# Kernel optimization log

Hardware: AMD Instinct MI355X
Metric: run time of the kernel (lower is better)

Reference implementation:

```python
import jax, jax.numpy as jnp
import numpy as np

BS, T, FIN, FOUT = 8, 1024, 512, 512
ALPHA = 0.1      # leaky relu slope
T_K = 3          # t_ksize (odd); temporal band radius = T_K // 2
S_K = 4          # s_ksize semantic topk
NEG_INF = -9e15


def setup_inputs() -> dict:
    key = jax.random.key(0)
    k1, k2, k3, k4 = jax.random.split(key, 4)
    # xavier-uniform-ish scales (gain 1.414)
    w_lim = 1.414 * np.sqrt(6.0 / (FIN + FOUT))
    a_lim = 1.414 * np.sqrt(6.0 / (2 * FOUT + 1))
    return {
        "x_a": jax.random.normal(k1, (BS, T, FIN), jnp.float32),
        "x_v": jax.random.normal(k2, (BS, T, FIN), jnp.float32),
        "W": jax.random.uniform(k3, (FIN, FOUT), jnp.float32, -w_lim, w_lim),
        "a": jax.random.uniform(k4, (2 * FOUT, 1), jnp.float32, -a_lim, a_lim),
    }


def _temporal_mask(t):
    # tem_adj[i,j] = 1 iff |i-j| <= T_K//2 and i, j on the same side of t-0.5
    idx = jnp.arange(2 * t)
    same_side = (idx[:, None] >= t) == (idx[None, :] >= t)
    band = jnp.abs(idx[:, None] - idx[None, :]) <= (T_K // 2)
    return band & same_side  # (2t, 2t) bool


def _semantic_block_mask(x, k):
    # x: (bs, t, d). Top-k neighbors by negative squared euclidean distance.
    inner = 2.0 * jnp.einsum("btd,bsd->bts", x, x)
    sq = jnp.sum(x * x, axis=-1, keepdims=True)  # (bs, t, 1)
    pd = -(sq - inner + jnp.swapaxes(sq, -1, -2))  # (bs, t, t)
    _, idx = jax.lax.top_k(pd, k)  # (bs, t, k)
    bs, t = x.shape[0], x.shape[1]
    b_ix = jnp.arange(bs)[:, None, None]
    r_ix = jnp.arange(t)[None, :, None]
    return jnp.zeros((bs, t, t), bool).at[b_ix, r_ix, idx].set(True)


def reference(x_a, x_v, W, a):
    bs, t, _ = x_a.shape
    h = jnp.concatenate([x_a, x_v], axis=1)          # (bs, 2t, FIN)
    Wh = h @ W                                        # (bs, 2t, FOUT)

    # additive GAT score: e = leakyrelu(Wh a1 + (Wh a2)^T)
    Wh1 = Wh @ a[:FOUT]                               # (bs, 2t, 1)
    Wh2 = Wh @ a[FOUT:]                               # (bs, 2t, 1)
    e = Wh1 + jnp.swapaxes(Wh2, -1, -2)               # (bs, 2t, 2t)
    e = jnp.where(e > 0, e, ALPHA * e)                # leaky relu

    # adjacency: temporal band + semantic topk within aa / vv blocks
    tem = _temporal_mask(t)                           # (2t, 2t)
    sem_aa = _semantic_block_mask(Wh[:, :t], S_K)     # (bs, t, t)
    sem_vv = _semantic_block_mask(Wh[:, t:], S_K)     # (bs, t, t)
    zb = jnp.zeros((bs, t, t), bool)
    sem = jnp.concatenate([
        jnp.concatenate([sem_aa, zb], axis=-1),
        jnp.concatenate([zb, sem_vv], axis=-1),
    ], axis=1)                                        # (bs, 2t, 2t)
    mask = tem[None] | sem

    attention = jax.nn.softmax(jnp.where(mask, e, NEG_INF), axis=-1)
    h_prime = jax.nn.elu(attention @ Wh)              # (bs, 2t, FOUT)
    return h_prime[:, :t], h_prime[:, t:]
```

## Files before the change

kernel.cpp:

```cpp
#include <hip/hip_runtime.h>
#include <math.h>

#define T_ 1024
#define BS_ 8
#define D_ 512
#define NROWS_ (BS_*2*T_)
#define ALPHA_ 0.1f

typedef _Float16 f16;
typedef _Float16 f16x8 __attribute__((ext_vector_type(8)));
typedef _Float16 f16x4 __attribute__((ext_vector_type(4)));
typedef _Float16 f16x2 __attribute__((ext_vector_type(2)));
typedef float f32x4 __attribute__((ext_vector_type(4)));

#define MFMA16(A,B,C) __builtin_amdgcn_mfma_f32_16x16x32_f16((A),(B),(C),0,0,0)

__device__ __forceinline__ void gl16(const void* g, void* l) {
    __builtin_amdgcn_global_load_lds(
        (const __attribute__((address_space(1))) unsigned int*)g,
        (__attribute__((address_space(3))) unsigned int*)l, 16, 0, 0);
}

#if __has_builtin(__builtin_amdgcn_fdot2)
__device__ __forceinline__ float fdot2p(f16x2 a, f16x2 b, float c) {
    return __builtin_amdgcn_fdot2(a, b, c, false);
}
#else
__device__ __forceinline__ float fdot2p(f16x2 a, f16x2 b, float c) {
    return fmaf((float)a[1], (float)b[1], fmaf((float)a[0], (float)b[0], c));
}
#endif

__device__ __forceinline__ float fdot8(const f16x8 a, const f16x8 b, float s) {
    #pragma unroll
    for (int q = 0; q < 4; ++q) {
        f16x2 aa, bb;
        aa[0] = a[2*q]; aa[1] = a[2*q+1];
        bb[0] = b[2*q]; bb[1] = b[2*q+1];
        s = fdot2p(aa, bb, s);
    }
    return s;
}

__device__ __forceinline__ unsigned sortable(float f) {
    unsigned u = __float_as_uint(f);
    return u ^ ((u & 0x80000000u) ? 0xFFFFFFFFu : 0x80000000u);
}
__device__ __forceinline__ unsigned pack_key(float s, int col) {
    return (sortable(s) & 0xFFFFFC00u) | (unsigned)(1023 - col);
}

#define INSK4(K, X) { \
    bool g3 = (X) > K[3], g2 = (X) > K[2], g1 = (X) > K[1], g0 = (X) > K[0]; \
    K[3] = g2 ? K[2] : (g3 ? (X) : K[3]); \
    K[2] = g1 ? K[1] : (g2 ? (X) : K[2]); \
    K[1] = g0 ? K[0] : (g1 ? (X) : K[1]); \
    K[0] = g0 ? (X) : K[0]; }

#define INSK8(K, X) { \
    bool h7=(X)>K[7],h6=(X)>K[6],h5=(X)>K[5],h4=(X)>K[4]; \
    bool h3=(X)>K[3],h2=(X)>K[2],h1=(X)>K[1],h0=(X)>K[0]; \
    K[7]=h6?K[6]:(h7?(X):K[7]); K[6]=h5?K[5]:(h6?(X):K[6]); \
    K[5]=h4?K[4]:(h5?(X):K[5]); K[4]=h3?K[3]:(h4?(X):K[4]); \
    K[3]=h2?K[2]:(h3?(X):K[3]); K[2]=h1?K[1]:(h2?(X):K[2]); \
    K[1]=h0?K[0]:(h1?(X):K[1]); K[0]=h0?(X):K[0]; }

#define CEU(a,b) { unsigned mx_ = (a) > (b) ? (a) : (b); \
    unsigned mn_ = (a) > (b) ? (b) : (a); (a) = mx_; (b) = mn_; }

#define MERGE8(K, MSK) { \
    unsigned b0=__shfl_xor(K[0],MSK), b1=__shfl_xor(K[1],MSK), \
             b2=__shfl_xor(K[2],MSK), b3=__shfl_xor(K[3],MSK), \
             b4=__shfl_xor(K[4],MSK), b5=__shfl_xor(K[5],MSK), \
             b6=__shfl_xor(K[6],MSK), b7=__shfl_xor(K[7],MSK); \
    K[0]=K[0]>b7?K[0]:b7; K[1]=K[1]>b6?K[1]:b6; \
    K[2]=K[2]>b5?K[2]:b5; K[3]=K[3]>b4?K[3]:b4; \
    K[4]=K[4]>b3?K[4]:b3; K[5]=K[5]>b2?K[5]:b2; \
    K[6]=K[6]>b1?K[6]:b1; K[7]=K[7]>b0?K[7]:b0; \
    CEU(K[0],K[4]); CEU(K[1],K[5]); CEU(K[2],K[6]); CEU(K[3],K[7]); \
    CEU(K[0],K[2]); CEU(K[1],K[3]); CEU(K[4],K[6]); CEU(K[5],K[7]); \
    CEU(K[0],K[1]); CEU(K[2],K[3]); CEU(K[4],K[5]); CEU(K[6],K[7]); }

#define BETTER(x,xi,v,vi) ((x) > (v) || ((x) == (v) && (xi) < (vi)))
#define INS4T(TV,TI,X,ID) { \
    bool g3 = BETTER(X,ID,TV[3],TI[3]), g2 = BETTER(X,ID,TV[2],TI[2]); \
    bool g1 = BETTER(X,ID,TV[1],TI[1]), g0 = BETTER(X,ID,TV[0],TI[0]); \
    TV[3] = g2 ? TV[2] : (g3 ? (X) : TV[3]); TI[3] = g2 ? TI[2] : (g3 ? (ID) : TI[3]); \
    TV[2] = g1 ? TV[1] : (g2 ? (X) : TV[2]); TI[2] = g1 ? TI[1] : (g2 ? (ID) : TI[2]); \
    TV[1] = g0 ? TV[0] : (g1 ? (X) : TV[1]); TI[1] = g0 ? TI[0] : (g1 ? (ID) : TI[1]); \
    TV[0] = g0 ? (X) : TV[0]; TI[0] = g0 ? (ID) : TI[0]; }

__global__ __launch_bounds__(256) void k_splitW(
    const float* __restrict__ W, f16* __restrict__ WTh, f16* __restrict__ WTl)
{
    __shared__ float tile[64][65];
    const int tid = threadIdx.x;
    const int tk = (blockIdx.x >> 3) << 6, tn = (blockIdx.x & 7) << 6;
    const int r0 = tid >> 4, c4 = (tid & 15) << 2;

    #pragma unroll
    for (int rr = 0; rr < 4; ++rr) {
        int k = r0 + (rr << 4);
        float4 v = *(const float4*)(W + (size_t)(tk + k) * D_ + tn + c4);
        tile[k][c4+0] = v.x; tile[k][c4+1] = v.y;
        tile[k][c4+2] = v.z; tile[k][c4+3] = v.w;
    }
    __syncthreads();
    #pragma unroll
    for (int rr = 0; rr < 4; ++rr) {
        int n = r0 + (rr << 4);
        f16x4 h, l;
        #pragma unroll
        for (int i = 0; i < 4; ++i) {
            float x = tile[c4 + i][n];
            f16 hh = (f16)x; h[i] = hh; l[i] = (f16)(x - (float)hh);
        }
        *(f16x4*)(WTh + (size_t)(tn + n) * D_ + tk + c4) = h;
        *(f16x4*)(WTl + (size_t)(tn + n) * D_ + tk + c4) = l;
    }
}

__global__ __launch_bounds__(256, 2) void k_gemm_wh(
    const float* __restrict__ xa, const float* __restrict__ xv,
    const f16* __restrict__ WTh, const f16* __restrict__ WTl,
    const float* __restrict__ a,
    f16* __restrict__ Whh, f16* __restrict__ Whl,
    float* __restrict__ Wh1, float* __restrict__ Wh2, float* __restrict__ sq)
{
    __shared__ __align__(16) unsigned char smem[73728];

    const int tid  = threadIdx.x;
    const int wc   = tid >> 6;
    const int lane = tid & 63;
    const int l15  = lane & 15;
    const int g    = lane >> 4;
    const int bid  = blockIdx.x;
    const int swz  = ((bid & 7) << 6) + (bid >> 3);
    const int rowbase = swz << 5;

    const int qp = rowbase >> 10;
    const float* xsrc = ((qp & 1) ? xv : xa)
                      + (size_t)((qp >> 1) * 1024 + (rowbase & 1023)) * D_;

    const char* WThB = (const char*)WTh;
    const char* WTlB = (const char*)WTl;

    const int rowA = tid >> 3, c8 = tid & 7;
    const int aW = (rowA << 6) + ((((c8 >> 1) ^ ((rowA >> 1) & 3)) << 4)) + ((c8 & 1) << 3);

    const int swzx = (g ^ ((l15 >> 1) & 3)) << 4;
    const int ao0 = (l15 << 6) + swzx;
    const int ao1 = ao0 + 1024;
    const int bo0 = (((wc << 6) +  0 + l15) << 6) + swzx;
    const int bo1 = (((wc << 6) + 16 + l15) << 6) + swzx;
    const int bo2 = (((wc << 6) + 32 + l15) << 6) + swzx;
    const int bo3 = (((wc << 6) + 48 + l15) << 6) + swzx;

    #define STAGE_B(cq_, bufb_, kc_) { \
        _Pragma("unroll") \
        for (int pp_ = 0; pp_ < 4; ++pp_) { \
            const int s_ = tid + (pp_ << 8); \
            const int rs_ = s_ >> 2, cs_ = s_ & 3; \
            const int jb_ = cs_ ^ ((rs_ >> 1) & 3); \
            const size_t gb_ = ((size_t)(((cq_) << 8) + rs_) << 10) + ((size_t)(kc_) << 6) + (jb_ << 4); \
            gl16(WThB + gb_, smem + (bufb_) + (s_ << 4)); \
            gl16(WTlB + gb_, smem + (bufb_) + 16384 + (s_ << 4)); } }

    #define STAGE_A(kc_) { \
        float4 v_ = *(const float4*)(xsrc + (size_t)rowA * D_ + ((kc_) << 5) + (c8 << 2)); \
        float xs_[4] = {v_.x, v_.y, v_.z, v_.w}; \
        f16x4 h_, l_; \
        _Pragma("unroll") \
        for (int e_ = 0; e_ < 4; ++e_) { \
            f16 hh_ = (f16)xs_[e_]; h_[e_] = hh_; l_[e_] = (f16)(xs_[e_] - (float)hh_); } \
        const int ab_ = 65536 + (((kc_) & 1) << 12); \
        *(f16x4*)(smem + ab_ + aW)        = h_; \
        *(f16x4*)(smem + ab_ + 2048 + aW) = l_; }

    #define COMPUTE(ACC, BUFB, AB) { \
        f16x8 ah0 = *(const f16x8*)(smem + (AB) + ao0); \
        f16x8 ah1 = *(const f16x8*)(smem + (AB) + ao1); \
        f16x8 al0 = *(const f16x8*)(smem + (AB) + 2048 + ao0); \
        f16x8 al1 = *(const f16x8*)(smem + (AB) + 2048 + ao1); \
        f16x8 bh0 = *(const f16x8*)(smem + (BUFB) + bo0); \
        f16x8 bh1 = *(const f16x8*)(smem + (BUFB) + bo1); \
        f16x8 bh2 = *(const f16x8*)(smem + (BUFB) + bo2); \
        f16x8 bh3 = *(const f16x8*)(smem + (BUFB) + bo3); \
        f16x8 bl0 = *(const f16x8*)(smem + (BUFB) + 16384 + bo0); \
        f16x8 bl1 = *(const f16x8*)(smem + (BUFB) + 16384 + bo1); \
        f16x8 bl2 = *(const f16x8*)(smem + (BUFB) + 16384 + bo2); \
        f16x8 bl3 = *(const f16x8*)(smem + (BUFB) + 16384 + bo3); \
        ACC[0][0] = MFMA16(ah0, bh0, ACC[0][0]); \
        ACC[0][1] = MFMA16(ah0, bh1, ACC[0][1]); \
        ACC[0][2] = MFMA16(ah0, bh2, ACC[0][2]); \
        ACC[0][3] = MFMA16(ah0, bh3, ACC[0][3]); \
        ACC[1][0] = MFMA16(ah1, bh0, ACC[1][0]); \
        ACC[1][1] = MFMA16(ah1, bh1, ACC[1][1]); \
        ACC[1][2] = MFMA16(ah1, bh2, ACC[1][2]); \
        ACC[1][3] = MFMA16(ah1, bh3, ACC[1][3]); \
        ACC[0][0] = MFMA16(al0, bh0, ACC[0][0]); \
        ACC[0][1] = MFMA16(al0, bh1, ACC[0][1]); \
        ACC[0][2] = MFMA16(al0, bh2, ACC[0][2]); \
        ACC[0][3] = MFMA16(al0, bh3, ACC[0][3]); \
        ACC[1][0] = MFMA16(al1, bh0, ACC[1][0]); \
        ACC[1][1] = MFMA16(al1, bh1, ACC[1][1]); \
        ACC[1][2] = MFMA16(al1, bh2, ACC[1][2]); \
        ACC[1][3] = MFMA16(al1, bh3, ACC[1][3]); \
        ACC[0][0] = MFMA16(ah0, bl0, ACC[0][0]); \
        ACC[0][1] = MFMA16(ah0, bl1, ACC[0][1]); \
        ACC[0][2] = MFMA16(ah0, bl2, ACC[0][2]); \
        ACC[0][3] = MFMA16(ah0, bl3, ACC[0][3]); \
        ACC[1][0] = MFMA16(ah1, bl0, ACC[1][0]); \
        ACC[1][1] = MFMA16(ah1, bl1, ACC[1][1]); \
        ACC[1][2] = MFMA16(ah1, bl2, ACC[1][2]); \
        ACC[1][3] = MFMA16(ah1, bl3, ACC[1][3]); }

    f32x4 acc0[2][4], acc1[2][4];
    #pragma unroll
    for (int m = 0; m < 2; ++m)
        #pragma unroll
        for (int c = 0; c < 4; ++c) {
            acc0[m][c] = (f32x4){0.f,0.f,0.f,0.f};
            acc1[m][c] = (f32x4){0.f,0.f,0.f,0.f};
        }

    STAGE_A(0);
    STAGE_B(0, 0, 0);

    for (int kk = 0; kk < 16; ++kk) {
        const int ab = 65536 + ((kk & 1) << 12);
        __syncthreads();
        STAGE_B(1, 32768, kk);
        COMPUTE(acc0, 0, ab);
        __syncthreads();
        if (kk < 15) { STAGE_B(0, 0, kk + 1); STAGE_A(kk + 1); }
        COMPUTE(acc1, 32768, ab);
    }
    #undef STAGE_B
    #undef STAGE_A
    #undef COMPUTE

    __syncthreads();

    float st1[8], st2[8], stq[8];
    #pragma unroll
    for (int s = 0; s < 8; ++s) { st1[s] = 0.f; st2[s] = 0.f; stq[s] = 0.f; }

    #define EPI(ACC, CQ) { \
        _Pragma("unroll") \
        for (int c = 0; c < 4; ++c) { \
            const int col = ((CQ) << 8) + (wc << 6) + (c << 4) + l15; \
            const float a1 = a[col]; \
            const float a2 = a[512 + col]; \
            _Pragma("unroll") \
            for (int m = 0; m < 2; ++m) \
            _Pragma("unroll") \
            for (int j = 0; j < 4; ++j) { \
                const float v = ACC[m][c][j]; \
                const int slot = (m << 2) + j; \
                st1[slot] = fmaf(v, a1, st1[slot]); \
                st2[slot] = fmaf(v, a2, st2[slot]); \
                stq[slot] = fmaf(v, v,  stq[slot]); \
                f16 h = (f16)v; f16 l = (f16)(v - (float)h); \
                const size_t off = (size_t)(rowbase + (m << 4) + (g << 2) + j) * D_ + col; \
                Whh[off] = h; Whl[off] = l; \
            } } }

    EPI(acc0, 0);
    EPI(acc1, 1);
    #undef EPI

    #pragma unroll
    for (int mask = 1; mask < 16; mask <<= 1)
        #pragma unroll
        for (int s = 0; s < 8; ++s) {
            st1[s] += __shfl_xor(st1[s], mask);
            st2[s] += __shfl_xor(st2[s], mask);
            stq[s] += __shfl_xor(stq[s], mask);
        }
    if (l15 == 0) {
        #pragma unroll
        for (int s = 0; s < 8; ++s) {
            const int rl = ((s >> 2) << 4) + (g << 2) + (s & 3);
            float* sp = (float*)smem + ((rl << 2) + wc) * 3;
            sp[0] = st1[s]; sp[1] = st2[s]; sp[2] = stq[s];
        }
    }
    __syncthreads();
    if (tid < 32) {
        float s1 = 0.f, s2 = 0.f, s3 = 0.f;
        #pragma unroll
        for (int wv = 0; wv < 4; ++wv) {
            const float* sp = (const float*)smem + ((tid << 2) + wv) * 3;
            s1 += sp[0]; s2 += sp[1]; s3 += sp[2];
        }
        Wh1[rowbase + tid] = s1; Wh2[rowbase + tid] = s2; sq[rowbase + tid] = s3;
    }
}

__global__ __launch_bounds__(256, 2) void k_gram_topk8(
    const f16* __restrict__ Whh, const float* __restrict__ sq,
    int* __restrict__ topk8)
{
    __shared__ __align__(16) unsigned char smem[73728];

    const int bid = blockIdx.x;
    const int swz = ((bid & 7) << 6) + (bid >> 3);
    const int p   = swz >> 5;
    const int rt  = swz & 31;
    const int rowbase  = (p << 10) + (rt << 5);
    const int colPanel = p << 10;

    const int tid  = threadIdx.x;
    const int wc   = tid >> 6;
    const int lane = tid & 63;
    const int l15  = lane & 15;
    const int g    = lane >> 4;
    const int r8   = lane >> 3;
    const int k7   = lane & 7;
    const int sw2  = ((k7 ^ r8) << 4);
    const int q0x  = ((g ^ (lane & 7)) << 4);

    const int rowA = tid >> 3;
    const int k7A  = tid & 7;
    const int aswz = ((k7A ^ (rowA & 7)) << 4);

    const char* WB = (const char*)Whh;

    const int aoff0 = 32768 + ((0  + l15) << 7) + q0x;
    const int aoff1 = 32768 + ((16 + l15) << 7) + q0x;
    const int boff0 = (((wc << 6) +  0 + l15) << 7) + q0x;
    const int boff1 = (((wc << 6) + 16 + l15) << 7) + q0x;
    const int boff2 = (((wc << 6) + 32 + l15) << 7) + q0x;
    const int boff3 = (((wc << 6) + 48 + l15) << 7) + q0x;

    f32x4 acc[2][4];
    #pragma unroll
    for (int m = 0; m < 2; ++m)
        #pragma unroll
        for (int c = 0; c < 4; ++c) acc[m][c] = (f32x4){0.f,0.f,0.f,0.f};

    unsigned k4[8][4];
    #pragma unroll
    for (int s = 0; s < 8; ++s)
        #pragma unroll
        for (int q = 0; q < 4; ++q) k4[s][q] = 0u;

    #define STAGE_G(t) { \
        const int ct_ = (t) >> 3, kc_ = (t) & 7; \
        const int bufb_ = ((t) & 1) * 36864; \
        _Pragma("unroll") \
        for (int hp_ = 0; hp_ < 2; ++hp_) { \
            const int wv_ = wc + (hp_ << 2); \
            size_t gB_ = ((size_t)(colPanel + (ct_ << 8) + (wv_ << 5) + r8) << 10) + (kc_ << 7) + sw2; \
            int ldsB_ = bufb_ + (wv_ << 12) + (lane << 4); \
            _Pragma("unroll") \
            for (int j_ = 0; j_ < 4; ++j_) { \
                gl16(WB + gB_, smem + ldsB_); \
                gB_ += (size_t)8 << 10; ldsB_ += 1024; \
            } } \
        size_t gA_ = ((size_t)(rowbase + rowA) << 10) + (kc_ << 7) + aswz; \
        gl16(WB + gA_, smem + bufb_ + 32768 + (tid << 4)); \
    }

    STAGE_G(0);

    for (int t = 0; t < 32; ++t) {
        __syncthreads();
        if (t < 31) STAGE_G(t + 1);
        const int bufb = (t & 1) * 36864;

        #pragma unroll
        for (int s = 0; s < 2; ++s) {
            const int sx = s << 6;
            f16x8 a0 = *(const f16x8*)(smem + bufb + (aoff0 ^ sx));
            f16x8 a1 = *(const f16x8*)(smem + bufb + (aoff1 ^ sx));
            f16x8 b0 = *(const f16x8*)(smem + bufb + (boff0 ^ sx));
            f16x8 b1 = *(const f16x8*)(smem + bufb + (boff1 ^ sx));
            f16x8 b2 = *(const f16x8*)(smem + bufb + (boff2 ^ sx));
            f16x8 b3 = *(const f16x8*)(smem + bufb + (boff3 ^ sx));
            acc[0][0] = MFMA16(a0, b0, acc[0][0]);
            acc[0][1] = MFMA16(a0, b1, acc[0][1]);
            acc[0][2] = MFMA16(a0, b2, acc[0][2]);
            acc[0][3] = MFMA16(a0, b3, acc[0][3]);
            acc[1][0] = MFMA16(a1, b0, acc[1][0]);
            acc[1][1] = MFMA16(a1, b1, acc[1][1]);
            acc[1][2] = MFMA16(a1, b2, acc[1][2]);
            acc[1][3] = MFMA16(a1, b3, acc[1][3]);
        }

        if ((t & 7) == 7) {
            const int ct = t >> 3;
            #pragma unroll
            for (int c = 0; c < 4; ++c) {
                const int cl = (ct << 8) + (wc << 6) + (c << 4) + l15;
                const float sqc = sq[colPanel + cl];
                #pragma unroll
                for (int m = 0; m < 2; ++m)
                    #pragma unroll
                    for (int j = 0; j < 4; ++j) {
                        float sc = fmaf(2.f, acc[m][c][j], -sqc);
                        unsigned key = pack_key(sc, cl);
                        INSK4(k4[(m << 2) + j], key);
                    }
                acc[0][c] = (f32x4){0.f,0.f,0.f,0.f};
                acc[1][c] = (f32x4){0.f,0.f,0.f,0.f};
            }
        }
    }

    unsigned k8[8][8];
    #pragma unroll
    for (int s = 0; s < 8; ++s) {
        #pragma unroll
        for (int q = 0; q < 4; ++q) { k8[s][q] = k4[s][q]; k8[s][4 + q] = 0u; }
    }
    #pragma unroll
    for (int msk = 1; msk < 16; msk <<= 1) {
        #pragma unroll
        for (int s = 0; s < 8; ++s) { MERGE8(k8[s], msk); }
    }

    if (l15 == 0) {
        #pragma unroll
        for (int s = 0; s < 8; ++s) {
            const int row_local = ((s >> 2) << 4) + (g << 2) + (s & 3);
            const int off = (((row_local << 2) + wc) << 5);
            *(uint4*)(smem + off)      = make_uint4(k8[s][0], k8[s][1], k8[s][2], k8[s][3]);
            *(uint4*)(smem + off + 16) = make_uint4(k8[s][4], k8[s][5], k8[s][6], k8[s][7]);
        }
    }
    __syncthreads();
    if (tid < 32) {
        const unsigned* bp = (const unsigned*)smem + (tid << 5);
        unsigned kk[8];
        #pragma unroll
        for (int s = 0; s < 8; ++s) kk[s] = bp[s];
        #pragma unroll
        for (int wv = 1; wv < 4; ++wv)
            #pragma unroll
            for (int s = 0; s < 8; ++s) { unsigned x = bp[(wv << 3) + s]; INSK8(kk, x); }
        #pragma unroll
        for (int s = 0; s < 8; ++s)
            topk8[(((size_t)(rowbase + tid)) << 3) + s] = 1023 - (int)(kk[s] & 1023u);
    }
    #undef STAGE_G
}

__global__ __launch_bounds__(256) void k_rescore_agg(
    const f16* __restrict__ Whh, const f16* __restrict__ Whl,
    const float* __restrict__ Wh1, const float* __restrict__ Wh2,
    const float* __restrict__ sq, const int* __restrict__ topk8,
    float* __restrict__ out)
{
    const int bid = blockIdx.x;
    const int swz = ((bid & 7) << 9) + (bid >> 3);
    const int tid  = threadIdx.x;
    const int lane = tid & 63;
    const int r    = (swz << 2) + (tid >> 6);
    const int p    = r >> 10;
    const int i    = r & 1023;
    const int rb   = p << 10;

    const size_t ro = (size_t)r * D_ + (lane << 3);
    f16x8 ah = *(const f16x8*)(Whh + ro);
    f16x8 al = *(const f16x8*)(Whl + ro);

    int cid[8];
    {
        int4 t0 = *(const int4*)(topk8 + ((size_t)r << 3));
        int4 t1 = *(const int4*)(topk8 + ((size_t)r << 3) + 4);
        cid[0]=t0.x; cid[1]=t0.y; cid[2]=t0.z; cid[3]=t0.w;
        cid[4]=t1.x; cid[5]=t1.y; cid[6]=t1.z; cid[7]=t1.w;
    }

    float dp[8];
    #pragma unroll
    for (int c = 0; c < 8; ++c) {
        const size_t co = (size_t)(rb + cid[c]) * D_ + (lane << 3);
        f16x8 bh = *(const f16x8*)(Whh + co);
        f16x8 bl = *(const f16x8*)(Whl + co);
        float s = 0.f;
        s = fdot8(ah, bh, s);
        s = fdot8(ah, bl, s);
        s = fdot8(al, bh, s);
        dp[c] = s;
    }
    #pragma unroll
    for (int off = 32; off > 0; off >>= 1)
        #pragma unroll
        for (int c = 0; c < 8; ++c) dp[c] += __shfl_xor(dp[c], off);

    float tv[4] = {-3.4e38f,-3.4e38f,-3.4e38f,-3.4e38f};
    int   ti[4] = {0x7FFFFFFF,0x7FFFFFFF,0x7FFFFFFF,0x7FFFFFFF};
    #pragma unroll
    for (int c = 0; c < 8; ++c) {
        float sc = fmaf(2.f, dp[c], -sq[rb + cid[c]]);
        INS4T(tv, ti, sc, cid[c]);
    }

    const int  tM = i - 1, tC = i, tP = i + 1;
    const bool vM = (i > 0), vP = (i < T_ - 1);
    const int s0 = ti[0], s1 = ti[1], s2 = ti[2], s3 = ti[3];

    bool u0 = !((vM && s0 == tM) || (s0 == tC) || (vP && s0 == tP));
    bool u1 = !((vM && s1 == tM) || (s1 == tC) || (vP && s1 == tP));
    bool u2 = !((vM && s2 == tM) || (s2 == tC) || (vP && s2 == tP));
    bool u3 = !((vM && s3 == tM) || (s3 == tC) || (vP && s3 == tP));

    int  ci[7] = { vM ? tM : 0, tC, vP ? tP : 0, s0, s1, s2, s3 };
    bool cv[7] = { vM, true, vP, u0, u1, u2, u3 };

    const float e1 = Wh1[r];
    float ev[7];
    float m = -3.4e38f;
    #pragma unroll
    for (int q = 0; q < 7; ++q) {
        float e = e1 + Wh2[rb + ci[q]];
        e = (e > 0.f) ? e : ALPHA_ * e;
        e = cv[q] ? e : -3.4e38f;
        ev[q] = e;
        m = fmaxf(m, e);
    }
    float wsum = 0.f;
    #pragma unroll
    for (int q = 0; q < 7; ++q) {
        float wq = cv[q] ? expf(ev[q] - m) : 0.f;
        ev[q] = wq;
        wsum += wq;
    }
    #pragma unroll
    for (int q = 0; q < 7; ++q) ev[q] /= wsum;

    float A[8] = {0.f,0.f,0.f,0.f,0.f,0.f,0.f,0.f};
    #pragma unroll
    for (int q = 0; q < 7; ++q) {
        if (ev[q] > 0.f) {
            const float wq = ev[q];
            const size_t qo = (size_t)(rb + ci[q]) * D_ + (lane << 3);
            f16x8 vh = *(const f16x8*)(Whh + qo);
            f16x8 vl = *(const f16x8*)(Whl + qo);
            #pragma unroll
            for (int e = 0; e < 8; ++e) A[e] = fmaf(wq, (float)vh[e], A[e]);
            #pragma unroll
            for (int e = 0; e < 8; ++e) A[e] = fmaf(wq, (float)vl[e], A[e]);
        }
    }
    #pragma unroll
    for (int e = 0; e < 8; ++e)
        A[e] = (A[e] > 0.f) ? A[e] : expm1f(A[e]);

    const int blk = p & 1, b = p >> 1;
    float* dst = out + (size_t)blk * ((size_t)BS_ * T_ * D_)
               + ((size_t)((b << 10) + i)) * D_ + (lane << 3);
    *(float4*)(dst)     = make_float4(A[0], A[1], A[2], A[3]);
    *(float4*)(dst + 4) = make_float4(A[4], A[5], A[6], A[7]);
}

extern "C" void kernel_launch(void* const* d_in, const int* in_sizes, int n_in,
                              void* d_out, int out_size, void* d_ws, size_t ws_size,
                              hipStream_t stream)
{
    const float* xa = (const float*)d_in[0];
    const float* xv = (const float*)d_in[1];
    const float* W  = (const float*)d_in[2];
    const float* a  = (const float*)d_in[3];
    float* out = (float*)d_out;

    f16* Whh    = (f16*)d_ws;
    f16* Whl    = Whh + (size_t)NROWS_ * D_;
    f16* WTh    = Whl + (size_t)NROWS_ * D_;
    f16* WTl    = WTh + (size_t)D_ * D_;
    float* Wh1  = (float*)(WTl + (size_t)D_ * D_);
    float* Wh2  = Wh1 + NROWS_;
    float* sq   = Wh2 + NROWS_;
    int* topk8  = (int*)(sq + NROWS_);

    k_splitW     <<<dim3(64),   dim3(256), 0, stream>>>(W, WTh, WTl);
    k_gemm_wh    <<<dim3(512),  dim3(256), 0, stream>>>(xa, xv, WTh, WTl, a, Whh, Whl, Wh1, Wh2, sq);
    k_gram_topk8 <<<dim3(512),  dim3(256), 0, stream>>>(Whh, sq, topk8);
    k_rescore_agg<<<dim3(4096), dim3(256), 0, stream>>>(Whh, Whl, Wh1, Wh2, sq, topk8, out);
}
```

Measured before the change: 129.4 us.

## Deepen GEMM and gram kernels to 4-stage async LDS pipelines with vmcnt waits

Both the Wh GEMM and the gram/top-k kernel move from a double-buffered loop with full __syncthreads to a 4-buffer ring with three stages in flight, gated by partial s_waitcnt vmcnt plus a barrier. In the GEMM, the fp32 x tile is now loaded straight into LDS via global_load_lds and split into hi/lo fp16 at compute time, no longer staged through registers. LDS per block doubles to 144KB and launch bounds drop to one block per CU, giving up occupancy in exchange for deeper memory latency hiding. The hard-coded vmcnt counts must match the number of loads each stage issues.

```diff
diff --git a/kernel.cpp b/kernel.cpp
--- a/kernel.cpp
+++ b/kernel.cpp
@@ -90,6 +90,13 @@
     TV[1] = g0 ? TV[0] : (g1 ? (X) : TV[1]); TI[1] = g0 ? TI[0] : (g1 ? (ID) : TI[1]); \
     TV[0] = g0 ? (X) : TV[0]; TI[0] = g0 ? (ID) : TI[0]; }
 
+#define PIPE_WAIT18() { asm volatile("s_waitcnt vmcnt(18)" ::: "memory"); \
+    __builtin_amdgcn_s_barrier(); __builtin_amdgcn_sched_barrier(0); }
+#define PIPE_WAIT9()  { asm volatile("s_waitcnt vmcnt(9)"  ::: "memory"); \
+    __builtin_amdgcn_s_barrier(); __builtin_amdgcn_sched_barrier(0); }
+#define PIPE_WAIT0()  { asm volatile("s_waitcnt vmcnt(0)"  ::: "memory"); \
+    __builtin_amdgcn_s_barrier(); __builtin_amdgcn_sched_barrier(0); }
+
 __global__ __launch_bounds__(256) void k_splitW(
     const float* __restrict__ W, f16* __restrict__ WTh, f16* __restrict__ WTl)
 {
@@ -120,14 +127,14 @@
     }
 }
 
-__global__ __launch_bounds__(256, 2) void k_gemm_wh(
+__global__ __launch_bounds__(256, 1) void k_gemm_wh(
     const float* __restrict__ xa, const float* __restrict__ xv,
     const f16* __restrict__ WTh, const f16* __restrict__ WTl,
     const float* __restrict__ a,
     f16* __restrict__ Whh, f16* __restrict__ Whl,
     float* __restrict__ Wh1, float* __restrict__ Wh2, float* __restrict__ sq)
 {
-    __shared__ __align__(16) unsigned char smem[73728];
+    __shared__ __align__(16) unsigned char smem[147456];
 
     const int tid  = threadIdx.x;
     const int wc   = tid >> 6;
@@ -141,47 +148,42 @@
     const int qp = rowbase >> 10;
     const float* xsrc = ((qp & 1) ? xv : xa)
                       + (size_t)((qp >> 1) * 1024 + (rowbase & 1023)) * D_;
+    const char* xsrcB = (const char*)xsrc;
 
     const char* WThB = (const char*)WTh;
     const char* WTlB = (const char*)WTl;
 
-    const int rowA = tid >> 3, c8 = tid & 7;
-    const int aW = (rowA << 6) + ((((c8 >> 1) ^ ((rowA >> 1) & 3)) << 4)) + ((c8 & 1) << 3);
-
     const int swzx = (g ^ ((l15 >> 1) & 3)) << 4;
-    const int ao0 = (l15 << 6) + swzx;
-    const int ao1 = ao0 + 1024;
     const int bo0 = (((wc << 6) +  0 + l15) << 6) + swzx;
     const int bo1 = (((wc << 6) + 16 + l15) << 6) + swzx;
     const int bo2 = (((wc << 6) + 32 + l15) << 6) + swzx;
     const int bo3 = (((wc << 6) + 48 + l15) << 6) + swzx;
-
-    #define STAGE_B(cq_, bufb_, kc_) { \
+    const int ar0 = (l15 << 7) + ((g ^ ((l15 >> 1) & 3)) << 5);
+
+    const int rA = tid >> 3, cA = tid & 7;
+    const int jcA = (((cA >> 1) ^ ((rA >> 1) & 3)) << 1) | (cA & 1);
+    const size_t gaA_base = (size_t)rA * 2048 + (jcA << 4);
+
+    #define STAGE(tau_) { \
+        const int cq_ = (tau_) & 1, kc_ = (tau_) >> 1; \
+        const int bufb_ = ((tau_) & 3) * 36864; \
         _Pragma("unroll") \
         for (int pp_ = 0; pp_ < 4; ++pp_) { \
             const int s_ = tid + (pp_ << 8); \
             const int rs_ = s_ >> 2, cs_ = s_ & 3; \
             const int jb_ = cs_ ^ ((rs_ >> 1) & 3); \
-            const size_t gb_ = ((size_t)(((cq_) << 8) + rs_) << 10) + ((size_t)(kc_) << 6) + (jb_ << 4); \
-            gl16(WThB + gb_, smem + (bufb_) + (s_ << 4)); \
-            gl16(WTlB + gb_, smem + (bufb_) + 16384 + (s_ << 4)); } }
-
-    #define STAGE_A(kc_) { \
-        float4 v_ = *(const float4*)(xsrc + (size_t)rowA * D_ + ((kc_) << 5) + (c8 << 2)); \
-        float xs_[4] = {v_.x, v_.y, v_.z, v_.w}; \
-        f16x4 h_, l_; \
+            const size_t gb_ = ((size_t)((cq_ << 8) + rs_) << 10) + ((size_t)kc_ << 6) + (jb_ << 4); \
+            gl16(WThB + gb_, smem + bufb_ + (s_ << 4)); \
+            gl16(WTlB + gb_, smem + bufb_ + 16384 + (s_ << 4)); } \
+        gl16(xsrcB + gaA_base + ((size_t)kc_ << 7), smem + bufb_ + 32768 + (tid << 4)); }
+
+    #define CONVA(H, L, p0, p1) { \
+        float xs_[8] = {p0[0],p0[1],p0[2],p0[3],p1[0],p1[1],p1[2],p1[3]}; \
         _Pragma("unroll") \
-        for (int e_ = 0; e_ < 4; ++e_) { \
-            f16 hh_ = (f16)xs_[e_]; h_[e_] = hh_; l_[e_] = (f16)(xs_[e_] - (float)hh_); } \
-        const int ab_ = 65536 + (((kc_) & 1) << 12); \
-        *(f16x4*)(smem + ab_ + aW)        = h_; \
-        *(f16x4*)(smem + ab_ + 2048 + aW) = l_; }
-
-    #define COMPUTE(ACC, BUFB, AB) { \
-        f16x8 ah0 = *(const f16x8*)(smem + (AB) + ao0); \
-        f16x8 ah1 = *(const f16x8*)(smem + (AB) + ao1); \
-        f16x8 al0 = *(const f16x8*)(smem + (AB) + 2048 + ao0); \
-        f16x8 al1 = *(const f16x8*)(smem + (AB) + 2048 + ao1); \
+        for (int e_ = 0; e_ < 8; ++e_) { \
+            f16 hh_ = (f16)xs_[e_]; H[e_] = hh_; L[e_] = (f16)(xs_[e_] - (float)hh_); } }
+
+    #define COMPUTE(ACC, BUFB) { \
         f16x8 bh0 = *(const f16x8*)(smem + (BUFB) + bo0); \
         f16x8 bh1 = *(const f16x8*)(smem + (BUFB) + bo1); \
         f16x8 bh2 = *(const f16x8*)(smem + (BUFB) + bo2); \
@@ -190,30 +192,44 @@
         f16x8 bl1 = *(const f16x8*)(smem + (BUFB) + 16384 + bo1); \
         f16x8 bl2 = *(const f16x8*)(smem + (BUFB) + 16384 + bo2); \
         f16x8 bl3 = *(const f16x8*)(smem + (BUFB) + 16384 + bo3); \
-        ACC[0][0] = MFMA16(ah0, bh0, ACC[0][0]); \
-        ACC[0][1] = MFMA16(ah0, bh1, ACC[0][1]); \
-        ACC[0][2] = MFMA16(ah0, bh2, ACC[0][2]); \
-        ACC[0][3] = MFMA16(ah0, bh3, ACC[0][3]); \
-        ACC[1][0] = MFMA16(ah1, bh0, ACC[1][0]); \
-        ACC[1][1] = MFMA16(ah1, bh1, ACC[1][1]); \
-        ACC[1][2] = MFMA16(ah1, bh2, ACC[1][2]); \
-        ACC[1][3] = MFMA16(ah1, bh3, ACC[1][3]); \
-        ACC[0][0] = MFMA16(al0, bh0, ACC[0][0]); \
-        ACC[0][1] = MFMA16(al0, bh1, ACC[0][1]); \
-        ACC[0][2] = MFMA16(al0, bh2, ACC[0][2]); \
-        ACC[0][3] = MFMA16(al0, bh3, ACC[0][3]); \
-        ACC[1][0] = MFMA16(al1, bh0, ACC[1][0]); \
-        ACC[1][1] = MFMA16(al1, bh1, ACC[1][1]); \
-        ACC[1][2] = MFMA16(al1, bh2, ACC[1][2]); \
-        ACC[1][3] = MFMA16(al1, bh3, ACC[1][3]); \
-        ACC[0][0] = MFMA16(ah0, bl0, ACC[0][0]); \
-        ACC[0][1] = MFMA16(ah0, bl1, ACC[0][1]); \
-        ACC[0][2] = MFMA16(ah0, bl2, ACC[0][2]); \
-        ACC[0][3] = MFMA16(ah0, bl3, ACC[0][3]); \
-        ACC[1][0] = MFMA16(ah1, bl0, ACC[1][0]); \
-        ACC[1][1] = MFMA16(ah1, bl1, ACC[1][1]); \
-        ACC[1][2] = MFMA16(ah1, bl2, ACC[1][2]); \
-        ACC[1][3] = MFMA16(ah1, bl3, ACC[1][3]); }
+        ACC[0][0] = MFMA16(AH0, bh0, ACC[0][0]); \
+        ACC[0][1] = MFMA16(AH0, bh1, ACC[0][1]); \
+        ACC[0][2] = MFMA16(AH0, bh2, ACC[0][2]); \
+        ACC[0][3] = MFMA16(AH0, bh3, ACC[0][3]); \
+        ACC[1][0] = MFMA16(AH1, bh0, ACC[1][0]); \
+        ACC[1][1] = MFMA16(AH1, bh1, ACC[1][1]); \
+        ACC[1][2] = MFMA16(AH1, bh2, ACC[1][2]); \
+        ACC[1][3] = MFMA16(AH1, bh3, ACC[1][3]); \
+        ACC[0][0] = MFMA16(AL0, bh0, ACC[0][0]); \
+        ACC[0][1] = MFMA16(AL0, bh1, ACC[0][1]); \
+        ACC[0][2] = MFMA16(AL0, bh2, ACC[0][2]); \
+        ACC[0][3] = MFMA16(AL0, bh3, ACC[0][3]); \
+        ACC[1][0] = MFMA16(AL1, bh0, ACC[1][0]); \
+        ACC[1][1] = MFMA16(AL1, bh1, ACC[1][1]); \
+        ACC[1][2] = MFMA16(AL1, bh2, ACC[1][2]); \
+        ACC[1][3] = MFMA16(AL1, bh3, ACC[1][3]); \
+        ACC[0][0] = MFMA16(AH0, bl0, ACC[0][0]); \
+        ACC[0][1] = MFMA16(AH0, bl1, ACC[0][1]); \
+        ACC[0][2] = MFMA16(AH0, bl2, ACC[0][2]); \
+        ACC[0][3] = MFMA16(AH0, bl3, ACC[0][3]); \
+        ACC[1][0] = MFMA16(AH1, bl0, ACC[1][0]); \
+        ACC[1][1] = MFMA16(AH1, bl1, ACC[1][1]); \
+        ACC[1][2] = MFMA16(AH1, bl2, ACC[1][2]); \
+        ACC[1][3] = MFMA16(AH1, bl3, ACC[1][3]); }
+
+    #define STEP(t_) { \
+        const int bufb = ((t_) & 3) * 36864; \
+        if (!((t_) & 1)) { \
+            f32x4 u0 = *(const f32x4*)(smem + bufb + 32768 + ar0); \
+            f32x4 u1 = *(const f32x4*)(smem + bufb + 32768 + ar0 + 16); \
+            f32x4 v0 = *(const f32x4*)(smem + bufb + 32768 + ar0 + 2048); \
+            f32x4 v1 = *(const f32x4*)(smem + bufb + 32768 + ar0 + 2048 + 16); \
+            CONVA(AH0, AL0, u0, u1); \
+            CONVA(AH1, AL1, v0, v1); \
+            COMPUTE(acc0, bufb); \
+        } else { \
+            COMPUTE(acc1, bufb); \
+        } }
 
     f32x4 acc0[2][4], acc1[2][4];
     #pragma unroll
@@ -223,22 +239,23 @@
             acc0[m][c] = (f32x4){0.f,0.f,0.f,0.f};
             acc1[m][c] = (f32x4){0.f,0.f,0.f,0.f};
         }
-
-    STAGE_A(0);
-    STAGE_B(0, 0, 0);
-
-    for (int kk = 0; kk < 16; ++kk) {
-        const int ab = 65536 + ((kk & 1) << 12);
-        __syncthreads();
-        STAGE_B(1, 32768, kk);
-        COMPUTE(acc0, 0, ab);
-        __syncthreads();
-        if (kk < 15) { STAGE_B(0, 0, kk + 1); STAGE_A(kk + 1); }
-        COMPUTE(acc1, 32768, ab);
-    }
-    #undef STAGE_B
-    #undef STAGE_A
+    f16x8 AH0, AH1, AL0, AL1;
+
+    STAGE(0); STAGE(1); STAGE(2);
+
+    for (int t = 0; t < 30; ++t) {
+        PIPE_WAIT18();
+        if (t < 29) STAGE(t + 3);
+        STEP(t);
+    }
+    PIPE_WAIT9();
+    STEP(30);
+    PIPE_WAIT0();
+    STEP(31);
+    #undef STAGE
+    #undef STEP
     #undef COMPUTE
+    #undef CONVA
 
     __syncthreads();
 
@@ -298,11 +315,11 @@
     }
 }
 
-__global__ __launch_bounds__(256, 2) void k_gram_topk8(
+__global__ __launch_bounds__(256, 1) void k_gram_topk8(
     const f16* __restrict__ Whh, const float* __restrict__ sq,
     int* __restrict__ topk8)
 {
-    __shared__ __align__(16) unsigned char smem[73728];
+    __shared__ __align__(16) unsigned char smem[147456];
 
     const int bid = blockIdx.x;
     const int swz = ((bid & 7) << 6) + (bid >> 3);
@@ -346,9 +363,9 @@
         #pragma unroll
         for (int q = 0; q < 4; ++q) k4[s][q] = 0u;
 
-    #define STAGE_G(t) { \
-        const int ct_ = (t) >> 3, kc_ = (t) & 7; \
-        const int bufb_ = ((t) & 1) * 36864; \
+    #define STAGE_G(tau_) { \
+        const int ct_ = (tau_) >> 3, kc_ = (tau_) & 7; \
+        const int bufb_ = ((tau_) & 3) * 36864; \
         _Pragma("unroll") \
         for (int hp_ = 0; hp_ < 2; ++hp_) { \
             const int wv_ = wc + (hp_ << 2); \
@@ -363,51 +380,57 @@
         gl16(WB + gA_, smem + bufb_ + 32768 + (tid << 4)); \
     }
 
-    STAGE_G(0);
-
-    for (int t = 0; t < 32; ++t) {
-        __syncthreads();
-        if (t < 31) STAGE_G(t + 1);
-        const int bufb = (t & 1) * 36864;
-
-        #pragma unroll
-        for (int s = 0; s < 2; ++s) {
-            const int sx = s << 6;
-            f16x8 a0 = *(const f16x8*)(smem + bufb + (aoff0 ^ sx));
-            f16x8 a1 = *(const f16x8*)(smem + bufb + (aoff1 ^ sx));
-            f16x8 b0 = *(const f16x8*)(smem + bufb + (boff0 ^ sx));
-            f16x8 b1 = *(const f16x8*)(smem + bufb + (boff1 ^ sx));
-            f16x8 b2 = *(const f16x8*)(smem + bufb + (boff2 ^ sx));
-            f16x8 b3 = *(const f16x8*)(smem + bufb + (boff3 ^ sx));
-            acc[0][0] = MFMA16(a0, b0, acc[0][0]);
-            acc[0][1] = MFMA16(a0, b1, acc[0][1]);
-            acc[0][2] = MFMA16(a0, b2, acc[0][2]);
-            acc[0][3] = MFMA16(a0, b3, acc[0][3]);
-            acc[1][0] = MFMA16(a1, b0, acc[1][0]);
-            acc[1][1] = MFMA16(a1, b1, acc[1][1]);
-            acc[1][2] = MFMA16(a1, b2, acc[1][2]);
-            acc[1][3] = MFMA16(a1, b3, acc[1][3]);
-        }
-
-        if ((t & 7) == 7) {
-            const int ct = t >> 3;
-            #pragma unroll
-            for (int c = 0; c < 4; ++c) {
-                const int cl = (ct << 8) + (wc << 6) + (c << 4) + l15;
-                const float sqc = sq[colPanel + cl];
-                #pragma unroll
-                for (int m = 0; m < 2; ++m)
-                    #pragma unroll
-                    for (int j = 0; j < 4; ++j) {
-                        float sc = fmaf(2.f, acc[m][c][j], -sqc);
-                        unsigned key = pack_key(sc, cl);
-                        INSK4(k4[(m << 2) + j], key);
-                    }
-                acc[0][c] = (f32x4){0.f,0.f,0.f,0.f};
-                acc[1][c] = (f32x4){0.f,0.f,0.f,0.f};
-            }
-        }
-    }
+    #define STEP_G(t_) { \
+        const int bufb = ((t_) & 3) * 36864; \
+        _Pragma("unroll") \
+        for (int s = 0; s < 2; ++s) { \
+            const int sx = s << 6; \
+            f16x8 a0 = *(const f16x8*)(smem + bufb + (aoff0 ^ sx)); \
+            f16x8 a1 = *(const f16x8*)(smem + bufb + (aoff1 ^ sx)); \
+            f16x8 b0 = *(const f16x8*)(smem + bufb + (boff0 ^ sx)); \
+            f16x8 b1 = *(const f16x8*)(smem + bufb + (boff1 ^ sx)); \
+            f16x8 b2 = *(const f16x8*)(smem + bufb + (boff2 ^ sx)); \
+            f16x8 b3 = *(const f16x8*)(smem + bufb + (boff3 ^ sx)); \
+            acc[0][0] = MFMA16(a0, b0, acc[0][0]); \
+            acc[0][1] = MFMA16(a0, b1, acc[0][1]); \
+            acc[0][2] = MFMA16(a0, b2, acc[0][2]); \
+            acc[0][3] = MFMA16(a0, b3, acc[0][3]); \
+            acc[1][0] = MFMA16(a1, b0, acc[1][0]); \
+            acc[1][1] = MFMA16(a1, b1, acc[1][1]); \
+            acc[1][2] = MFMA16(a1, b2, acc[1][2]); \
+            acc[1][3] = MFMA16(a1, b3, acc[1][3]); \
+        } \
+        if (((t_) & 7) == 7) { \
+            const int ct = (t_) >> 3; \
+            _Pragma("unroll") \
+            for (int c = 0; c < 4; ++c) { \
+                const int cl = (ct << 8) + (wc << 6) + (c << 4) + l15; \
+                const float sqc = sq[colPanel + cl]; \
+                _Pragma("unroll") \
+                for (int m = 0; m < 2; ++m) \
+                _Pragma("unroll") \
+                for (int j = 0; j < 4; ++j) { \
+                    float sc = fmaf(2.f, acc[m][c][j], -sqc); \
+                    unsigned key = pack_key(sc, cl); \
+                    INSK4(k4[(m << 2) + j], key); \
+                } \
+                acc[0][c] = (f32x4){0.f,0.f,0.f,0.f}; \
+                acc[1][c] = (f32x4){0.f,0.f,0.f,0.f}; \
+            } } }
+
+    STAGE_G(0); STAGE_G(1); STAGE_G(2);
+
+    for (int t = 0; t < 30; ++t) {
+        PIPE_WAIT18();
+        if (t < 29) STAGE_G(t + 3);
+        STEP_G(t);
+    }
+    PIPE_WAIT9();
+    STEP_G(30);
+    PIPE_WAIT0();
+    STEP_G(31);
+    #undef STAGE_G
+    #undef STEP_G
 
     unsigned k8[8][8];
     #pragma unroll
@@ -421,6 +444,7 @@
         for (int s = 0; s < 8; ++s) { MERGE8(k8[s], msk); }
     }
 
+    __syncthreads();
     if (l15 == 0) {
         #pragma unroll
         for (int s = 0; s < 8; ++s) {
@@ -444,7 +468,6 @@
         for (int s = 0; s < 8; ++s)
             topk8[(((size_t)(rowbase + tid)) << 3) + s] = 1023 - (int)(kk[s] & 1023u);
     }
-    #undef STAGE_G
 }
 
 __global__ __launch_bounds__(256) void k_rescore_agg(
```

New measurement: 161.5 us. 24.8% more time.
